# Kernel optimization log

Hardware: AMD Instinct MI355X
Metric: run time of the kernel (lower is better)

The kernel has to match this reference:

```python
import jax, jax.numpy as jnp
import numpy as np

B, D, H, W = 2, 16, 16, 16
N = D * H * W
CDESC = 64
TEMP = 0.07
TOPK = 24
RADIUS = 0.45


def flatten_spatial(x):
    # (B, C, D, H, W) -> (B, N, C)
    b, c = x.shape[:2]
    return x.reshape(b, c, -1).transpose(0, 2, 1)


def voxel_grid():
    # normalized voxel-center grid in [-1, 1], shape (3, D, H, W)
    zs = jnp.linspace(-1.0, 1.0, D)
    ys = jnp.linspace(-1.0, 1.0, H)
    xs = jnp.linspace(-1.0, 1.0, W)
    return jnp.stack(jnp.meshgrid(zs, ys, xs, indexing='ij'), axis=0)


def setup_inputs() -> dict:
    key = jax.random.key(0)
    ks = jax.random.split(key, 8)
    return {
        'src_canonical': jax.random.normal(ks[0], (B, 3, D, H, W), jnp.float32),
        'tgt_canonical': jax.random.normal(ks[1], (B, 3, D, H, W), jnp.float32),
        'src_desc': jax.random.normal(ks[2], (B, CDESC, D, H, W), jnp.float32),
        'tgt_desc': jax.random.normal(ks[3], (B, CDESC, D, H, W), jnp.float32),
        'src_mlogits': jax.random.normal(ks[4], (B, 2, D, H, W), jnp.float32),
        'tgt_mlogits': jax.random.normal(ks[5], (B, 2, D, H, W), jnp.float32),
        'src_unc': jax.random.uniform(ks[6], (B, 1, D, H, W), jnp.float32),
        'tgt_unc': jax.random.uniform(ks[7], (B, 1, D, H, W), jnp.float32),
    }


def reference(src_canonical, tgt_canonical, src_desc, tgt_desc,
              src_mlogits, tgt_mlogits, src_unc, tgt_unc):
    sc = flatten_spatial(src_canonical)  # (B, N, 3)
    tc = flatten_spatial(tgt_canonical)  # (B, N, 3)
    sd = flatten_spatial(src_desc)       # (B, N, C)
    td = flatten_spatial(tgt_desc)       # (B, N, C)

    # torch.cdist: Euclidean distance matrix (B, N, N)
    d2 = (jnp.sum(sc * sc, -1)[:, :, None]
          + jnp.sum(tc * tc, -1)[:, None, :]
          - 2.0 * jnp.einsum('bid,bjd->bij', sc, tc))
    dist = jnp.sqrt(jnp.maximum(d2, 1e-12))

    sim = jnp.einsum('bid,bjd->bij', sd, td)  # (B, N, N)

    k = min(TOPK, N)
    _, nn_idx = jax.lax.top_k(-dist, k)  # k smallest distances per row
    bidx = jnp.arange(B)[:, None, None]
    ridx = jnp.arange(N)[None, :, None]
    allowed = jnp.zeros((B, N, N), bool).at[bidx, ridx, nn_idx].set(True)
    allowed = allowed | (dist <= RADIUS)

    tgt_match = jax.nn.softmax(flatten_spatial(tgt_mlogits), axis=-1)[..., 0]  # (B, N)
    src_match = jax.nn.softmax(flatten_spatial(src_mlogits), axis=-1)[..., 0]  # (B, N)

    # (B, N, 1) + (B, 1, N) rank-1 uncertainty penalty
    unc = flatten_spatial(src_unc) + flatten_spatial(tgt_unc).transpose(0, 2, 1)

    scores = sim - dist - 0.1 * unc
    scores = jnp.where(allowed, scores, -10000.0)
    # legacy matchability score mode
    scores = scores + jnp.maximum(jnp.log(tgt_match), -20.0)[:, None, :]
    probs = jax.nn.softmax(scores / TEMP, axis=-1)
    probs = jnp.nan_to_num(probs, nan=0.0, posinf=0.0, neginf=0.0)

    tpos = voxel_grid().reshape(3, -1).T  # (N, 3)
    expected = jnp.einsum('bij,jd->bid', probs, tpos)  # (B, N, 3)
    src_pos = jnp.broadcast_to(tpos, (B, N, 3))

    disp = (expected - src_pos).transpose(0, 2, 1).reshape(B, 3, D, H, W)
    disp = jnp.nan_to_num(disp, nan=0.0, posinf=0.0, neginf=0.0)

    conf = (jnp.max(probs, axis=-1) * src_match).reshape(B, 1, D, H, W)

    ent = -jnp.sum(probs * jnp.log(jnp.clip(probs, 1e-12, None)), axis=-1)
    ent = jnp.nan_to_num(ent, nan=0.0, posinf=0.0, neginf=0.0).reshape(B, 1, D, H, W)

    return expected, disp, probs, conf, ent, src_pos
```

## Files before the change

### kernel.cpp

```cpp
#include <hip/hip_runtime.h>
#include <math.h>
#include <stddef.h>

#define NN    4096
#define BATCH 2
#define CD    64
#define KSEL  24
#define LCAP  1024
#define RAD2  0.2025f

__device__ __forceinline__ int blk_sum_i(int v, int* buf) {
#pragma unroll
  for (int off = 32; off; off >>= 1) v += __shfl_down(v, off);
  __syncthreads();
  if ((threadIdx.x & 63) == 0) buf[threadIdx.x >> 6] = v;
  __syncthreads();
  return buf[0] + buf[1] + buf[2] + buf[3];
}

__global__ __launch_bounds__(256)
void prep_all(const float* __restrict__ td, const float* __restrict__ sd,
              const float* __restrict__ tml, const float* __restrict__ tu,
              float* __restrict__ tdT, float* __restrict__ sdT,
              float* __restrict__ addj) {
  __shared__ float tile[64][65];
  int blk = blockIdx.x;
  if (blk < 256) {
    const float* src = (blk < 128) ? td  : sd;
    float*       dst = (blk < 128) ? tdT : sdT;
    int lb = blk & 127;
    int b  = lb >> 6;
    int j0 = (lb & 63) << 6;
    int jl = threadIdx.x & 63;
    int cq = threadIdx.x >> 6;
    const float* srcp = src + (size_t)b * CD * NN;
#pragma unroll
    for (int r = 0; r < 16; ++r) {
      int c = r * 4 + cq;
      tile[c][jl] = srcp[(size_t)c * NN + j0 + jl];
    }
    __syncthreads();
    float* dstp = dst + (size_t)b * NN * CD;
#pragma unroll
    for (int r = 0; r < 16; ++r) {
      int j = r * 4 + cq;
      dstp[(size_t)(j0 + j) * CD + jl] = tile[jl][j];
    }
  } else {
    int idx = (blk - 256) * 256 + threadIdx.x;
    if (idx < BATCH * NN) {
      int b = idx >> 12, j = idx & (NN - 1);
      float l0 = tml[(size_t)b * 2 * NN + j];
      float l1 = tml[(size_t)b * 2 * NN + NN + j];
      float x  = l1 - l0;
      float sp = fmaxf(x, 0.0f) + log1pf(expf(-fabsf(x)));
      addj[idx] = fmaxf(-sp, -20.0f) - 0.1f * tu[idx];
    }
  }
}

__global__ __launch_bounds__(256)
void matcher_main(const float* __restrict__ sc, const float* __restrict__ tc,
                  const float* __restrict__ sd, const float* __restrict__ td,
                  const float* __restrict__ tdT, const float* __restrict__ sdT,
                  const float* __restrict__ addj,
                  const float* __restrict__ tml, const float* __restrict__ tu,
                  const float* __restrict__ sml,
                  float* __restrict__ oexp, float* __restrict__ odisp,
                  float* __restrict__ oprob, float* __restrict__ oconf,
                  float* __restrict__ oent, float* __restrict__ osrc) {
  __shared__ float4 sdp4[CD / 4];
  __shared__ float  scv[3];
  __shared__ __align__(16) int hist[1024];
  __shared__ float  cand[128];
  __shared__ int    candn;
  __shared__ int    sBin, sBelow;
  __shared__ float  sD24;
  __shared__ int    ibuf[4];
  __shared__ int    jlist[LCAP];
  __shared__ float  vlist[LCAP];
  __shared__ int    lcount;

  const int tid = threadIdx.x;
  const int row = blockIdx.x;
  const int b   = row >> 12;
  const int i   = row & (NN - 1);

  if (sdT) {
    if (tid < CD / 4) sdp4[tid] = ((const float4*)(sdT + ((size_t)b * NN + i) * CD))[tid];
  } else {
    if (tid < CD) ((float*)sdp4)[tid] = sd[(size_t)b * CD * NN + (size_t)tid * NN + i];
  }
  if (tid >= 64 && tid < 67) scv[tid - 64] = sc[(size_t)b * 3 * NN + (size_t)(tid - 64) * NN + i];
  ((int4*)hist)[tid] = make_int4(0, 0, 0, 0);
  if (tid == 0) { candn = 0; lcount = 0; sBin = -1; }
  __syncthreads();

  const float s0 = scv[0], s1 = scv[1], s2 = scv[2];
  const float ssq = s0 * s0 + s1 * s1 + s2 * s2;

  const float4* tcx = (const float4*)(tc + (size_t)b * 3 * NN);
  const float4* tcy = tcx + NN / 4;
  const float4* tcz = tcy + NN / 4;

  float d2v[4][4];
#pragma unroll
  for (int k = 0; k < 4; ++k) {
    int g = tid + 256 * k;
    float4 X = tcx[g], Y = tcy[g], Z = tcz[g];
    float xx[4] = {X.x, X.y, X.z, X.w};
    float yy[4] = {Y.x, Y.y, Y.z, Y.w};
    float zz[4] = {Z.x, Z.y, Z.z, Z.w};
#pragma unroll
    for (int r = 0; r < 4; ++r) {
      float t0 = xx[r], t1 = yy[r], t2 = zz[r];
      float tsq = t0 * t0 + t1 * t1 + t2 * t2;
      float dot = s0 * t0 + s1 * t1 + s2 * t2;
      float d2  = fmaxf(ssq + tsq - 2.0f * dot, 1e-12f);
      d2v[k][r] = d2;
      if (d2 < 1.0f) atomicAdd(&hist[(int)(d2 * 1024.0f)], 1);
    }
  }

  {
    float4* prow = (float4*)(oprob + (size_t)row * NN);
    float4 z4; z4.x = z4.y = z4.z = z4.w = 0.0f;
#pragma unroll
    for (int k = 0; k < 4; ++k) prow[tid + 256 * k] = z4;
  }
  __syncthreads();

  {
    int4 h4 = ((int4*)hist)[tid];
    int loc = h4.x + h4.y + h4.z + h4.w;
    int pre = loc;
#pragma unroll
    for (int off = 1; off < 64; off <<= 1) {
      int q = __shfl_up(pre, off);
      if ((tid & 63) >= off) pre += q;
    }
    if ((tid & 63) == 63) ibuf[tid >> 6] = pre;
    __syncthreads();
    int wbase = 0;
#pragma unroll
    for (int w = 0; w < 4; ++w) wbase += (w < (tid >> 6)) ? ibuf[w] : 0;
    int below = wbase + pre - loc;
    int hh[4] = {h4.x, h4.y, h4.z, h4.w};
#pragma unroll
    for (int q = 0; q < 4; ++q) {
      if (below < KSEL && below + hh[q] >= KSEL) { sBin = 4 * tid + q; sBelow = below; }
      below += hh[q];
    }
    __syncthreads();
  }
  const int Bstar = sBin;
  const int cb    = sBelow;
  bool fb = (Bstar < 0);

  if (!fb) {
#pragma unroll
    for (int k = 0; k < 4; ++k)
#pragma unroll
      for (int r = 0; r < 4; ++r) {
        float d2 = d2v[k][r];
        if (d2 < 1.0f && (int)(d2 * 1024.0f) == Bstar) {
          int idx = atomicAdd(&candn, 1);
          if (idx < 128) cand[idx] = d2;
        }
      }
    __syncthreads();
    if (candn > 128) fb = true;
  }
  if (!fb) {
    int nc = candn, Krem = KSEL - cb;
    if (tid < nc) {
      float v = cand[tid];
      int lt = 0, le = 0;
      for (int m2 = 0; m2 < nc; ++m2) { float u = cand[m2]; lt += (u < v); le += (u <= v); }
      if (lt < Krem && le >= Krem) sD24 = v;
    }
  } else {
    unsigned lo = 0u, hi = 0x7F800000u;
    while (lo < hi) {
      unsigned mid = (lo + hi) >> 1;
      int c = 0;
#pragma unroll
      for (int k = 0; k < 4; ++k)
#pragma unroll
        for (int r = 0; r < 4; ++r) c += (__float_as_uint(d2v[k][r]) <= mid);
      c = blk_sum_i(c, ibuf);
      if (c >= KSEL) hi = mid; else lo = mid + 1;
    }
    if (tid == 0) sD24 = __uint_as_float(lo);
  }
  __syncthreads();
  const float thr2 = fmaxf(sD24, RAD2);

#pragma unroll
  for (int k = 0; k < 4; ++k) {
    int g = tid + 256 * k;
#pragma unroll
    for (int r = 0; r < 4; ++r) {
      float d2 = d2v[k][r];
      if (d2 <= thr2) {
        int idx = atomicAdd(&lcount, 1);
        if (idx < LCAP) { jlist[idx] = 4 * g + r; vlist[idx] = d2; }
      }
    }
  }
  __syncthreads();
  const int na = lcount < LCAP ? lcount : LCAP;

  if (tid >= 64) return;

  const float* tdb = tdT ? tdT + (size_t)b * NN * CD : nullptr;
  float mloc = -1e30f;
  for (int e = tid; e < na; e += 64) {
    int j   = jlist[e];
    float d2 = vlist[e];
    float sim = 0.0f;
    if (tdb) {
      const float4* trow = (const float4*)(tdb + (size_t)j * CD);
#pragma unroll
      for (int q = 0; q < CD / 4; ++q) {
        float4 a = sdp4[q], t = trow[q];
        sim = fmaf(a.x, t.x, fmaf(a.y, t.y, fmaf(a.z, t.z, fmaf(a.w, t.w, sim))));
      }
    } else {
      const float* spx = (const float*)sdp4;
      const float* tp  = td + (size_t)b * CD * NN + j;
#pragma unroll 8
      for (int c = 0; c < CD; ++c) sim = fmaf(spx[c], tp[(size_t)c * NN], sim);
    }
    float aj;
    if (addj) {
      aj = addj[(size_t)b * NN + j];
    } else {
      float l0 = tml[(size_t)b * 2 * NN + j];
      float l1 = tml[(size_t)b * 2 * NN + NN + j];
      float x  = l1 - l0;
      float sp = fmaxf(x, 0.0f) + log1pf(expf(-fabsf(x)));
      aj = fmaxf(-sp, -20.0f) - 0.1f * tu[(size_t)b * NN + j];
    }
    float s = sim - sqrtf(d2) + aj;
    vlist[e] = s;
    mloc = fmaxf(mloc, s);
  }
#pragma unroll
  for (int off = 32; off; off >>= 1) mloc = fmaxf(mloc, __shfl_xor(mloc, off));
  const float m = mloc;

  const float C1 = (1.0f / 0.07f) * 1.44269504089f;
  float zl = 0.0f, evu = 0.0f, evm = 0.0f;
  for (int e = tid; e < na; e += 64) {
    float u  = (vlist[e] - m) * C1;
    float ev = exp2f(u);
    vlist[e] = ev;
    zl  += ev;
    evu  = fmaf(ev, u, evu);
    evm  = fmaxf(evm, ev);
  }
#pragma unroll
  for (int off = 32; off; off >>= 1) {
    zl  += __shfl_xor(zl, off);
    evu += __shfl_xor(evu, off);
    evm  = fmaxf(evm, __shfl_xor(evm, off));
  }
  const float Z = zl, invZ = 1.0f / zl;

  const float STEP = 2.0f / 15.0f;
  float ex0 = 0.f, ex1 = 0.f, ex2 = 0.f;
  for (int e = tid; e < na; e += 64) {
    float p = vlist[e] * invZ;
    int j = jlist[e];
    oprob[(size_t)row * NN + j] = p;
    float pz = -1.0f + STEP * (float)(j >> 8);
    float py = -1.0f + STEP * (float)((j >> 4) & 15);
    float px = -1.0f + STEP * (float)(j & 15);
    ex0 = fmaf(p, pz, ex0); ex1 = fmaf(p, py, ex1); ex2 = fmaf(p, px, ex2);
  }
#pragma unroll
  for (int off = 32; off; off >>= 1) {
    ex0 += __shfl_xor(ex0, off);
    ex1 += __shfl_xor(ex1, off);
    ex2 += __shfl_xor(ex2, off);
  }

  if (tid == 0) {
    const float LN2 = 0.69314718056f;
    float ent = LN2 * (log2f(Z) - evu * invZ);
    float tz = -1.0f + STEP * (float)(i >> 8);
    float ty = -1.0f + STEP * (float)((i >> 4) & 15);
    float tx = -1.0f + STEP * (float)(i & 15);
    size_t r3 = (size_t)row * 3;
    oexp[r3 + 0] = ex0; oexp[r3 + 1] = ex1; oexp[r3 + 2] = ex2;
    osrc[r3 + 0] = tz;  osrc[r3 + 1] = ty;  osrc[r3 + 2] = tx;
    size_t db = (size_t)b * 3 * NN;
    odisp[db + 0 * NN + i] = ex0 - tz;
    odisp[db + 1 * NN + i] = ex1 - ty;
    odisp[db + 2 * NN + i] = ex2 - tx;
    float ls0 = sml[(size_t)b * 2 * NN + i];
    float ls1 = sml[(size_t)b * 2 * NN + NN + i];
    float smv = 1.0f / (1.0f + expf(ls1 - ls0));
    oconf[(size_t)b * NN + i] = (evm * invZ) * smv;
    oent[(size_t)b * NN + i]  = ent;
  }
}

extern "C" void kernel_launch(void* const* d_in, const int* in_sizes, int n_in,
                              void* d_out, int out_size, void* d_ws, size_t ws_size,
                              hipStream_t stream) {
  const float* sc  = (const float*)d_in[0];
  const float* tc  = (const float*)d_in[1];
  const float* sd  = (const float*)d_in[2];
  const float* td  = (const float*)d_in[3];
  const float* sml = (const float*)d_in[4];
  const float* tml = (const float*)d_in[5];
  const float* tu  = (const float*)d_in[7];

  float* out   = (float*)d_out;
  float* oexp  = out;
  float* odisp = oexp  + (size_t)BATCH * NN * 3;
  float* oprob = odisp + (size_t)BATCH * NN * 3;
  float* oconf = oprob + (size_t)BATCH * NN * NN;
  float* oent  = oconf + (size_t)BATCH * NN;
  float* osrc  = oent  + (size_t)BATCH * NN;

  size_t need = ((size_t)2 * BATCH * NN * CD + (size_t)BATCH * NN) * sizeof(float);
  float* tdT = nullptr;
  float* sdT = nullptr;
  float* adj = nullptr;
  if (ws_size >= need) {
    tdT = (float*)d_ws;
    sdT = tdT + (size_t)BATCH * NN * CD;
    adj = sdT + (size_t)BATCH * NN * CD;
    prep_all<<<256 + 32, 256, 0, stream>>>(td, sd, tml, tu, tdT, sdT, adj);
  }
  matcher_main<<<BATCH * NN, 256, 0, stream>>>(sc, tc, sd, td, tdT, sdT, adj,
                                               tml, tu, sml,
                                               oexp, odisp, oprob, oconf, oent, osrc);
}
```

Measured before the change: 221.4 us.

## Process one row per wavefront with float-bit histogram and two-pass selection

Each 64-lane wavefront now handles a whole row independently (four rows per block), replacing block-wide __syncthreads with wave-local fences and ballot/shuffle reductions. Top-k selection uses a 256-bin histogram keyed on float exponent/mantissa bits, then a second distance pass collects the candidates and the selected list together, replacing the register-held distances and the binary-search fallback. Work per row moves from 256 threads to 64, and shared buffers shrink so more blocks fit per CU. The risk is that the fixed caps (128 candidates, 256 selected) can overflow on adversarial inputs, and distances are now computed twice per row.

```diff
diff --git a/kernel.cpp b/kernel.cpp
--- a/kernel.cpp
+++ b/kernel.cpp
@@ -6,16 +6,15 @@
 #define BATCH 2
 #define CD    64
 #define KSEL  24
-#define LCAP  1024
 #define RAD2  0.2025f
-
-__device__ __forceinline__ int blk_sum_i(int v, int* buf) {
-#pragma unroll
-  for (int off = 32; off; off >>= 1) v += __shfl_down(v, off);
-  __syncthreads();
-  if ((threadIdx.x & 63) == 0) buf[threadIdx.x >> 6] = v;
-  __syncthreads();
-  return buf[0] + buf[1] + buf[2] + buf[3];
+#define NBINS 256
+#define KBASE 1888
+#define CCAP  128
+#define LCAP  256
+
+__device__ __forceinline__ int d2key(float d2) {
+  int k = (int)(__float_as_uint(d2) >> 19) - KBASE;
+  return k < 0 ? 0 : (k > NBINS - 1 ? NBINS - 1 : k);
 }
 
 __global__ __launch_bounds__(256)
@@ -59,7 +58,7 @@
   }
 }
 
-__global__ __launch_bounds__(256)
+__global__ __launch_bounds__(256, 6)
 void matcher_main(const float* __restrict__ sc, const float* __restrict__ tc,
                   const float* __restrict__ sd, const float* __restrict__ td,
                   const float* __restrict__ tdT, const float* __restrict__ sdT,
@@ -69,155 +68,126 @@
                   float* __restrict__ oexp, float* __restrict__ odisp,
                   float* __restrict__ oprob, float* __restrict__ oconf,
                   float* __restrict__ oent, float* __restrict__ osrc) {
-  __shared__ float4 sdp4[CD / 4];
-  __shared__ float  scv[3];
-  __shared__ __align__(16) int hist[1024];
-  __shared__ float  cand[128];
-  __shared__ int    candn;
-  __shared__ int    sBin, sBelow;
-  __shared__ float  sD24;
-  __shared__ int    ibuf[4];
-  __shared__ int    jlist[LCAP];
-  __shared__ float  vlist[LCAP];
-  __shared__ int    lcount;
-
-  const int tid = threadIdx.x;
-  const int row = blockIdx.x;
-  const int b   = row >> 12;
-  const int i   = row & (NN - 1);
-
-  if (sdT) {
-    if (tid < CD / 4) sdp4[tid] = ((const float4*)(sdT + ((size_t)b * NN + i) * CD))[tid];
-  } else {
-    if (tid < CD) ((float*)sdp4)[tid] = sd[(size_t)b * CD * NN + (size_t)tid * NN + i];
-  }
-  if (tid >= 64 && tid < 67) scv[tid - 64] = sc[(size_t)b * 3 * NN + (size_t)(tid - 64) * NN + i];
-  ((int4*)hist)[tid] = make_int4(0, 0, 0, 0);
-  if (tid == 0) { candn = 0; lcount = 0; sBin = -1; }
-  __syncthreads();
-
-  const float s0 = scv[0], s1 = scv[1], s2 = scv[2];
-  const float ssq = s0 * s0 + s1 * s1 + s2 * s2;
+  __shared__ __align__(16) int   hist[4][NBINS];
+  __shared__ __align__(16) float sdp[4][CD];
+  __shared__ float cand_d[4][CCAP];
+  __shared__ int   cand_j[4][CCAP];
+  __shared__ int   jlist[4][LCAP];
+  __shared__ float vlist[4][LCAP];
+  __shared__ int   candn[4], lcount[4];
+  __shared__ float sD24[4];
+
+  const int tid  = threadIdx.x;
+  const int w    = tid >> 6;
+  const int lane = tid & 63;
+  const int row  = blockIdx.x * 4 + w;
+  const int b    = row >> 12;
+  const int i    = row & (NN - 1);
+
+  ((int4*)hist[w])[lane] = make_int4(0, 0, 0, 0);
+  if (lane == 0) { candn[w] = 0; lcount[w] = 0; }
+  if (sdT) sdp[w][lane] = sdT[((size_t)b * NN + i) * CD + lane];
+  else     sdp[w][lane] = sd[(size_t)b * CD * NN + (size_t)lane * NN + i];
+  const float s0 = sc[(size_t)b * 3 * NN + i];
+  const float s1 = sc[(size_t)b * 3 * NN + NN + i];
+  const float s2 = sc[(size_t)b * 3 * NN + 2 * NN + i];
+  __threadfence_block();
 
   const float4* tcx = (const float4*)(tc + (size_t)b * 3 * NN);
   const float4* tcy = tcx + NN / 4;
   const float4* tcz = tcy + NN / 4;
-
-  float d2v[4][4];
-#pragma unroll
-  for (int k = 0; k < 4; ++k) {
-    int g = tid + 256 * k;
+  float4* prow4 = (float4*)(oprob + (size_t)row * NN);
+  float4 z4; z4.x = z4.y = z4.z = z4.w = 0.0f;
+
+#pragma unroll 4
+  for (int k = 0; k < 16; ++k) {
+    int g = (k << 6) + lane;
     float4 X = tcx[g], Y = tcy[g], Z = tcz[g];
-    float xx[4] = {X.x, X.y, X.z, X.w};
-    float yy[4] = {Y.x, Y.y, Y.z, Y.w};
-    float zz[4] = {Z.x, Z.y, Z.z, Z.w};
+    prow4[g] = z4;
+    float xs[4] = {X.x, X.y, X.z, X.w};
+    float ys[4] = {Y.x, Y.y, Y.z, Y.w};
+    float zs[4] = {Z.x, Z.y, Z.z, Z.w};
 #pragma unroll
     for (int r = 0; r < 4; ++r) {
-      float t0 = xx[r], t1 = yy[r], t2 = zz[r];
-      float tsq = t0 * t0 + t1 * t1 + t2 * t2;
-      float dot = s0 * t0 + s1 * t1 + s2 * t2;
-      float d2  = fmaxf(ssq + tsq - 2.0f * dot, 1e-12f);
-      d2v[k][r] = d2;
-      if (d2 < 1.0f) atomicAdd(&hist[(int)(d2 * 1024.0f)], 1);
-    }
-  }
-
-  {
-    float4* prow = (float4*)(oprob + (size_t)row * NN);
-    float4 z4; z4.x = z4.y = z4.z = z4.w = 0.0f;
-#pragma unroll
-    for (int k = 0; k < 4; ++k) prow[tid + 256 * k] = z4;
-  }
-  __syncthreads();
-
-  {
-    int4 h4 = ((int4*)hist)[tid];
-    int loc = h4.x + h4.y + h4.z + h4.w;
-    int pre = loc;
-#pragma unroll
-    for (int off = 1; off < 64; off <<= 1) {
-      int q = __shfl_up(pre, off);
-      if ((tid & 63) >= off) pre += q;
-    }
-    if ((tid & 63) == 63) ibuf[tid >> 6] = pre;
-    __syncthreads();
-    int wbase = 0;
-#pragma unroll
-    for (int w = 0; w < 4; ++w) wbase += (w < (tid >> 6)) ? ibuf[w] : 0;
-    int below = wbase + pre - loc;
-    int hh[4] = {h4.x, h4.y, h4.z, h4.w};
-#pragma unroll
-    for (int q = 0; q < 4; ++q) {
-      if (below < KSEL && below + hh[q] >= KSEL) { sBin = 4 * tid + q; sBelow = below; }
-      below += hh[q];
-    }
-    __syncthreads();
-  }
-  const int Bstar = sBin;
-  const int cb    = sBelow;
-  bool fb = (Bstar < 0);
-
-  if (!fb) {
-#pragma unroll
-    for (int k = 0; k < 4; ++k)
-#pragma unroll
-      for (int r = 0; r < 4; ++r) {
-        float d2 = d2v[k][r];
-        if (d2 < 1.0f && (int)(d2 * 1024.0f) == Bstar) {
-          int idx = atomicAdd(&candn, 1);
-          if (idx < 128) cand[idx] = d2;
-        }
+      float dx = xs[r] - s0, dy = ys[r] - s1, dz = zs[r] - s2;
+      float d2 = fmaxf(__fmaf_rn(dx, dx, __fmaf_rn(dy, dy, dz * dz)), 1e-12f);
+      atomicAdd(&hist[w][d2key(d2)], 1);
+    }
+  }
+  __threadfence_block();
+
+  int4 h4 = ((int4*)hist[w])[lane];
+  int hv[4] = {h4.x, h4.y, h4.z, h4.w};
+  int s = hv[0] + hv[1] + hv[2] + hv[3];
+  int inc = s;
+#pragma unroll
+  for (int off = 1; off < 64; off <<= 1) {
+    int t = __shfl_up(inc, off);
+    if (lane >= off) inc += t;
+  }
+  int pre = inc - s;
+  int Bl = -1, Bb = 0, below = pre;
+#pragma unroll
+  for (int q = 0; q < 4; ++q) {
+    if (Bl < 0 && below < KSEL && below + hv[q] >= KSEL) { Bl = 4 * lane + q; Bb = below; }
+    below += hv[q];
+  }
+  unsigned long long mk = __ballot(Bl >= 0);
+  int srcl = __ffsll(mk) - 1;
+  const int Bstar = __shfl(Bl, srcl);
+  const int cb    = __shfl(Bb, srcl);
+  const int Krem  = KSEL - cb;
+  if (lane == 0) sD24[w] = __uint_as_float((unsigned)(Bstar + KBASE + 1) << 19);
+
+#pragma unroll 4
+  for (int k = 0; k < 16; ++k) {
+    int g = (k << 6) + lane;
+    float4 X = tcx[g], Y = tcy[g], Z = tcz[g];
+    float xs[4] = {X.x, X.y, X.z, X.w};
+    float ys[4] = {Y.x, Y.y, Y.z, Y.w};
+    float zs[4] = {Z.x, Z.y, Z.z, Z.w};
+#pragma unroll
+    for (int r = 0; r < 4; ++r) {
+      float dx = xs[r] - s0, dy = ys[r] - s1, dz = zs[r] - s2;
+      float d2 = fmaxf(__fmaf_rn(dx, dx, __fmaf_rn(dy, dy, dz * dz)), 1e-12f);
+      int key = d2key(d2);
+      int j = (g << 2) + r;
+      if (key == Bstar) {
+        int c = atomicAdd(&candn[w], 1);
+        if (c < CCAP) { cand_d[w][c] = d2; cand_j[w][c] = j; }
+      } else if (key < Bstar || d2 <= RAD2) {
+        int c = atomicAdd(&lcount[w], 1);
+        if (c < LCAP) { jlist[w][c] = j; vlist[w][c] = d2; }
       }
-    __syncthreads();
-    if (candn > 128) fb = true;
-  }
-  if (!fb) {
-    int nc = candn, Krem = KSEL - cb;
-    if (tid < nc) {
-      float v = cand[tid];
-      int lt = 0, le = 0;
-      for (int m2 = 0; m2 < nc; ++m2) { float u = cand[m2]; lt += (u < v); le += (u <= v); }
-      if (lt < Krem && le >= Krem) sD24 = v;
-    }
-  } else {
-    unsigned lo = 0u, hi = 0x7F800000u;
-    while (lo < hi) {
-      unsigned mid = (lo + hi) >> 1;
-      int c = 0;
-#pragma unroll
-      for (int k = 0; k < 4; ++k)
-#pragma unroll
-        for (int r = 0; r < 4; ++r) c += (__float_as_uint(d2v[k][r]) <= mid);
-      c = blk_sum_i(c, ibuf);
-      if (c >= KSEL) hi = mid; else lo = mid + 1;
-    }
-    if (tid == 0) sD24 = __uint_as_float(lo);
-  }
-  __syncthreads();
-  const float thr2 = fmaxf(sD24, RAD2);
-
-#pragma unroll
-  for (int k = 0; k < 4; ++k) {
-    int g = tid + 256 * k;
-#pragma unroll
-    for (int r = 0; r < 4; ++r) {
-      float d2 = d2v[k][r];
-      if (d2 <= thr2) {
-        int idx = atomicAdd(&lcount, 1);
-        if (idx < LCAP) { jlist[idx] = 4 * g + r; vlist[idx] = d2; }
-      }
-    }
-  }
-  __syncthreads();
-  const int na = lcount < LCAP ? lcount : LCAP;
-
-  if (tid >= 64) return;
+    }
+  }
+  __threadfence_block();
+
+  int nc = candn[w]; nc = nc > CCAP ? CCAP : nc;
+  for (int e = lane; e < nc; e += 64) {
+    float v = cand_d[w][e];
+    int lt = 0, le = 0;
+    for (int m = 0; m < nc; ++m) { float u = cand_d[w][m]; lt += (u < v); le += (u <= v); }
+    if (lt < Krem && le >= Krem) sD24[w] = v;
+  }
+  __threadfence_block();
+  const float thr2 = fmaxf(sD24[w], RAD2);
+  for (int e = lane; e < nc; e += 64) {
+    float v = cand_d[w][e];
+    if (v <= thr2) {
+      int c = atomicAdd(&lcount[w], 1);
+      if (c < LCAP) { jlist[w][c] = cand_j[w][e]; vlist[w][c] = v; }
+    }
+  }
+  __threadfence_block();
+  int na = lcount[w]; na = na > LCAP ? LCAP : na;
 
   const float* tdb = tdT ? tdT + (size_t)b * NN * CD : nullptr;
+  const float4* sdp4 = (const float4*)sdp[w];
   float mloc = -1e30f;
-  for (int e = tid; e < na; e += 64) {
-    int j   = jlist[e];
-    float d2 = vlist[e];
+  for (int e = lane; e < na; e += 64) {
+    int j = jlist[w][e];
+    float d2 = vlist[w][e];
     float sim = 0.0f;
     if (tdb) {
       const float4* trow = (const float4*)(tdb + (size_t)j * CD);
@@ -242,9 +212,9 @@
       float sp = fmaxf(x, 0.0f) + log1pf(expf(-fabsf(x)));
       aj = fmaxf(-sp, -20.0f) - 0.1f * tu[(size_t)b * NN + j];
     }
-    float s = sim - sqrtf(d2) + aj;
-    vlist[e] = s;
-    mloc = fmaxf(mloc, s);
+    float sco = sim - sqrtf(d2) + aj;
+    vlist[w][e] = sco;
+    mloc = fmaxf(mloc, sco);
   }
 #pragma unroll
   for (int off = 32; off; off >>= 1) mloc = fmaxf(mloc, __shfl_xor(mloc, off));
@@ -252,10 +222,10 @@
 
   const float C1 = (1.0f / 0.07f) * 1.44269504089f;
   float zl = 0.0f, evu = 0.0f, evm = 0.0f;
-  for (int e = tid; e < na; e += 64) {
-    float u  = (vlist[e] - m) * C1;
+  for (int e = lane; e < na; e += 64) {
+    float u  = (vlist[w][e] - m) * C1;
     float ev = exp2f(u);
-    vlist[e] = ev;
+    vlist[w][e] = ev;
     zl  += ev;
     evu  = fmaf(ev, u, evu);
     evm  = fmaxf(evm, ev);
@@ -268,11 +238,13 @@
   }
   const float Z = zl, invZ = 1.0f / zl;
 
+  __builtin_amdgcn_s_waitcnt(0x0F70);
+
   const float STEP = 2.0f / 15.0f;
   float ex0 = 0.f, ex1 = 0.f, ex2 = 0.f;
-  for (int e = tid; e < na; e += 64) {
-    float p = vlist[e] * invZ;
-    int j = jlist[e];
+  for (int e = lane; e < na; e += 64) {
+    float p = vlist[w][e] * invZ;
+    int j = jlist[w][e];
     oprob[(size_t)row * NN + j] = p;
     float pz = -1.0f + STEP * (float)(j >> 8);
     float py = -1.0f + STEP * (float)((j >> 4) & 15);
@@ -286,7 +258,7 @@
     ex2 += __shfl_xor(ex2, off);
   }
 
-  if (tid == 0) {
+  if (lane == 0) {
     const float LN2 = 0.69314718056f;
     float ent = LN2 * (log2f(Z) - evu * invZ);
     float tz = -1.0f + STEP * (float)(i >> 8);
@@ -336,7 +308,7 @@
     adj = sdT + (size_t)BATCH * NN * CD;
     prep_all<<<256 + 32, 256, 0, stream>>>(td, sd, tml, tu, tdT, sdT, adj);
   }
-  matcher_main<<<BATCH * NN, 256, 0, stream>>>(sc, tc, sd, td, tdT, sdT, adj,
-                                               tml, tu, sml,
-                                               oexp, odisp, oprob, oconf, oent, osrc);
+  matcher_main<<<BATCH * NN / 4, 256, 0, stream>>>(sc, tc, sd, td, tdT, sdT, adj,
+                                                   tml, tu, sml,
+                                                   oexp, odisp, oprob, oconf, oent, osrc);
 }
```

Measured after the change: 206.9 us. 6.5% less time.
